# Kernel optimization log

Hardware: AMD Instinct MI355X
Metric: run time of the kernel (lower is better)

The kernel has to match this reference:

```python
import jax, jax.numpy as jnp
import numpy as np

N = 100000
E = 800000
HID = 128
HEADS = 4
NEG_SLOPE = 0.2


def _mlp2(x, w1, b1, w2, b2):
    h = jax.nn.relu(x @ w1.T + b1)
    return jax.nn.relu(h @ w2.T + b2)


def gat_conv(h, src, dst, lin_w, att_src, att_dst, bias, heads, out_ch, concat):
    # h: [N, in] -> hl: [N, heads, out_ch]
    n = h.shape[0]
    hl = (h @ lin_w.T).reshape(n, heads, out_ch)
    a_s = jnp.sum(hl * att_src, axis=-1)  # [N, heads]
    a_d = jnp.sum(hl * att_dst, axis=-1)
    alpha = jax.nn.leaky_relu(a_s[src] + a_d[dst], NEG_SLOPE)  # [E', heads]
    amax = jax.ops.segment_max(alpha, dst, num_segments=n)
    ex = jnp.exp(alpha - amax[dst])
    denom = jax.ops.segment_sum(ex, dst, num_segments=n)
    att = ex / denom[dst]  # segment softmax over incoming edges
    msg = hl[src] * att[:, :, None]  # [E', heads, out_ch]
    out = jax.ops.segment_sum(msg, dst, num_segments=n)
    out = out.reshape(n, heads * out_ch) if concat else out.mean(axis=1)
    return out + bias


def setup_inputs() -> dict:
    key = jax.random.key(0)
    ks = iter(jax.random.split(key, 40))
    g = lambda shape: (jax.random.normal(next(ks), shape, dtype=jnp.float32) * 0.1)
    inp = {}
    inp['x'] = jax.random.normal(next(ks), (N, 2), dtype=jnp.float32)
    inp['node_types'] = jax.random.randint(next(ks), (N,), 0, 2, dtype=jnp.int32)
    inp['edge_index'] = jax.random.randint(next(ks), (2, E), 0, N, dtype=jnp.int64)
    # heterogeneous encoder
    inp['ew1'] = g((HID, 2)); inp['eb1'] = g((HID,))
    inp['ew2'] = g((HID, HID)); inp['eb2'] = g((HID,))
    inp['cw1'] = g((HID, 1)); inp['cb1'] = g((HID,))
    inp['cw2'] = g((HID, HID)); inp['cb2'] = g((HID,))
    # GAT layers 0,1: heads=4, out_ch=HID//4, concat
    C = HID // HEADS
    inp['lin0'] = g((HID, HID)); inp['as0'] = g((HEADS, C)); inp['ad0'] = g((HEADS, C)); inp['b0'] = g((HID,))
    inp['lin1'] = g((HID, HID)); inp['as1'] = g((HEADS, C)); inp['ad1'] = g((HEADS, C)); inp['b1'] = g((HID,))
    # GAT layer 2: heads=1, out_ch=HID, concat=False
    inp['lin2'] = g((HID, HID)); inp['as2'] = g((1, HID)); inp['ad2'] = g((1, HID)); inp['b2'] = g((HID,))
    # decoder
    inp['dw1'] = g((HID, HID)); inp['db1'] = g((HID,))
    inp['dw2'] = g((HID // 2, HID)); inp['db2'] = g((HID // 2,))
    inp['dw3'] = g((1, HID // 2)); inp['db3'] = g((1,))
    return inp


def reference(x, node_types, edge_index, ew1, eb1, ew2, eb2, cw1, cb1, cw2, cb2,
              lin0, as0, ad0, b0, lin1, as1, ad1, b1, lin2, as2, ad2, b2,
              dw1, db1, dw2, db2, dw3, db3):
    n = x.shape[0]
    # heterogeneous encoding (vectorized type select)
    item_h = _mlp2(x[:, :2], ew1, eb1, ew2, eb2)
    con_h = _mlp2(x[:, :1], cw1, cb1, cw2, cb2)
    item_mask = node_types == 0
    h = jnp.where(item_mask[:, None], item_h, jnp.where((node_types == 1)[:, None], con_h, 0.0))
    # add self-loops (PyG GATConv default add_self_loops=True)
    loop = jnp.arange(n, dtype=edge_index.dtype)
    src = jnp.concatenate([edge_index[0], loop])
    dst = jnp.concatenate([edge_index[1], loop])
    C = HID // HEADS
    h0 = jax.nn.relu(gat_conv(h, src, dst, lin0, as0, ad0, b0, HEADS, C, True))
    h1 = h0 + jax.nn.relu(gat_conv(h0, src, dst, lin1, as1, ad1, b1, HEADS, C, True))
    h2 = h1 + jax.nn.relu(gat_conv(h1, src, dst, lin2, as2, ad2, b2, 1, HID, False))
    # decoder on all nodes; zero out non-item nodes (dropout is eval/no-op)
    d = jax.nn.relu(h2 @ dw1.T + db1)
    d = jax.nn.relu(d @ dw2.T + db2)
    probs = jax.nn.sigmoid(d @ dw3.T + db3).squeeze(-1)
    return probs * item_mask.astype(probs.dtype)
```

## Files before the change

kernel.cpp:

```cpp
#include <hip/hip_runtime.h>
#include <math.h>

#define HIDDEN 128
#define NEG_SLOPE 0.2f

typedef unsigned short u16;
typedef __attribute__((ext_vector_type(8))) short bf16x8;
typedef __attribute__((ext_vector_type(4))) float f32x4;

__device__ __forceinline__ u16 f2bf(float f) {
    unsigned u = __float_as_uint(f);
    unsigned r = (u + 0x7FFFu + ((u >> 16) & 1u)) >> 16;
    return (u16)r;
}
__device__ __forceinline__ float bf2f(u16 u) {
    return __uint_as_float((unsigned)u << 16);
}
__device__ __forceinline__ unsigned pack2(float a, float b) {
    return (unsigned)f2bf(a) | ((unsigned)f2bf(b) << 16);
}
__device__ __forceinline__ float lo16f(unsigned v) { return bf2f((u16)v); }
__device__ __forceinline__ float hi16f(unsigned v) { return bf2f((u16)(v >> 16)); }

struct WPtrs { const float* p[7]; };
__global__ void convw_zero_kernel(WPtrs wp, unsigned* __restrict__ wb, int totalPairs,
                                  int* __restrict__ cnt, int N) {
    int i = blockIdx.x * blockDim.x + threadIdx.x;
    if (i < N) cnt[i] = 0;
    if (i < totalPairs) {
        int e = i * 2;
        int seg, off;
        if (e < 98304) { seg = e >> 14; off = e & 16383; }
        else           { seg = 6;       off = e - 98304; }
        const float* s = wp.p[seg];
        wb[i] = pack2(s[off], s[off + 1]);
    }
}

__global__ __launch_bounds__(256) void encoder_kernel(
        const float* __restrict__ x, const int* __restrict__ types,
        const float* __restrict__ ew1, const float* __restrict__ eb1,
        const float* __restrict__ cw1, const float* __restrict__ cb1,
        const u16* __restrict__ wb_ew2, const u16* __restrict__ wb_cw2,
        const float* __restrict__ eb2, const float* __restrict__ cb2,
        u16* __restrict__ out, int N) {
    __shared__ u16 Ws[128 * 136];
    __shared__ float xsh[128];
    __shared__ float w1sh[640];
    const int tid = threadIdx.x;
    const int n0 = blockIdx.x * 64;

    if (tid < 128) {
        int n = n0 + (tid >> 1);
        xsh[tid] = (n < N) ? x[2 * n + (tid & 1)] : 0.f;
    }
    if (tid < 256) w1sh[tid] = ew1[tid];
    if (tid < 128) { w1sh[256 + tid] = eb1[tid]; w1sh[384 + tid] = cw1[tid];
                     w1sh[512 + tid] = cb1[tid]; }
#pragma unroll
    for (int r = 0; r < 8; r++) {
        int j = r * 256 + tid;
        int row = j >> 4, c8 = (j & 15) << 3;
        *(uint4*)&Ws[row * 136 + c8] = *(const uint4*)&wb_ew2[(size_t)row * 128 + c8];
    }
    __syncthreads();

    const int w = tid >> 6, lane = tid & 63;
    const int qd = lane >> 4, lr = lane & 15;
    const int row = w * 16 + lr;
    const float x0 = xsh[2 * row], x1 = xsh[2 * row + 1];

    f32x4 acc_i[8], acc_c[8];
#pragma unroll
    for (int j = 0; j < 8; j++) acc_i[j] = (f32x4){0.f, 0.f, 0.f, 0.f};

#pragma unroll
    for (int k = 0; k < 4; k++) {
        bf16x8 a;
#pragma unroll
        for (int j = 0; j < 8; j++) {
            int t = k * 32 + qd * 8 + j;
            float v = fmaxf(w1sh[2 * t] * x0 + w1sh[2 * t + 1] * x1 + w1sh[256 + t], 0.f);
            a[j] = (short)f2bf(v);
        }
#pragma unroll
        for (int j = 0; j < 8; j++) {
            bf16x8 b = *(const bf16x8*)&Ws[(j * 16 + lr) * 136 + k * 32 + qd * 8];
            acc_i[j] = __builtin_amdgcn_mfma_f32_16x16x32_bf16(a, b, acc_i[j], 0, 0, 0);
        }
    }
    __syncthreads();

#pragma unroll
    for (int r = 0; r < 8; r++) {
        int j = r * 256 + tid;
        int rw = j >> 4, c8 = (j & 15) << 3;
        *(uint4*)&Ws[rw * 136 + c8] = *(const uint4*)&wb_cw2[(size_t)rw * 128 + c8];
    }
    __syncthreads();

#pragma unroll
    for (int j = 0; j < 8; j++) acc_c[j] = (f32x4){0.f, 0.f, 0.f, 0.f};
#pragma unroll
    for (int k = 0; k < 4; k++) {
        bf16x8 a;
#pragma unroll
        for (int j = 0; j < 8; j++) {
            int t = k * 32 + qd * 8 + j;
            float v = fmaxf(w1sh[384 + t] * x0 + w1sh[512 + t], 0.f);
            a[j] = (short)f2bf(v);
        }
#pragma unroll
        for (int j = 0; j < 8; j++) {
            bf16x8 b = *(const bf16x8*)&Ws[(j * 16 + lr) * 136 + k * 32 + qd * 8];
            acc_c[j] = __builtin_amdgcn_mfma_f32_16x16x32_bf16(a, b, acc_c[j], 0, 0, 0);
        }
    }

#pragma unroll
    for (int r = 0; r < 4; r++) {
        int orow = n0 + w * 16 + qd * 4 + r;
        if (orow >= N) continue;
        int ty = types[orow];
#pragma unroll
        for (int j = 0; j < 8; j++) {
            int col = j * 16 + lr;
            float v;
            if (ty == 0)      v = fmaxf(acc_i[j][r] + eb2[col], 0.f);
            else if (ty == 1) v = fmaxf(acc_c[j][r] + cb2[col], 0.f);
            else              v = 0.f;
            out[(size_t)orow * HIDDEN + col] = f2bf(v);
        }
    }
}

template <int OUT, int DH>
__global__ __launch_bounds__(256) void gemm_mfma_kernel(
        const u16* __restrict__ X, const u16* __restrict__ Wb,
        const float* __restrict__ bias, const int* __restrict__ types,
        u16* __restrict__ out, float* __restrict__ a_s, float* __restrict__ a_d,
        const float* __restrict__ att_s, const float* __restrict__ att_d,
        const float* __restrict__ dw3, const float* __restrict__ db3,
        float* __restrict__ fout, int N, int mode) {
    constexpr int NT = OUT / 16;
    __shared__ u16 Xs[64 * 136];
    __shared__ u16 Ws[OUT * 136];
    const int tid = threadIdx.x;
    const int n0 = blockIdx.x * 64;

#pragma unroll
    for (int r = 0; r < 4; r++) {
        int j = r * 256 + tid;
        int row = j >> 4, c8 = (j & 15) << 3;
        int n = n0 + row;
        uint4 v = make_uint4(0u, 0u, 0u, 0u);
        if (n < N) v = *(const uint4*)&X[(size_t)n * 128 + c8];
        *(uint4*)&Xs[row * 136 + c8] = v;
    }
#pragma unroll
    for (int r = 0; r < NT; r++) {
        int j = r * 256 + tid;
        int row = j >> 4, c8 = (j & 15) << 3;
        *(uint4*)&Ws[row * 136 + c8] = *(const uint4*)&Wb[(size_t)row * 128 + c8];
    }
    __syncthreads();

    const int w = tid >> 6, lane = tid & 63;
    const int qd = lane >> 4, lr = lane & 15;

    f32x4 acc[NT];
#pragma unroll
    for (int j = 0; j < NT; j++) acc[j] = (f32x4){0.f, 0.f, 0.f, 0.f};

#pragma unroll
    for (int k = 0; k < 4; k++) {
        bf16x8 a = *(const bf16x8*)&Xs[(w * 16 + lr) * 136 + k * 32 + qd * 8];
#pragma unroll
        for (int j = 0; j < NT; j++) {
            bf16x8 b = *(const bf16x8*)&Ws[(j * 16 + lr) * 136 + k * 32 + qd * 8];
            acc[j] = __builtin_amdgcn_mfma_f32_16x16x32_bf16(a, b, acc[j], 0, 0, 0);
        }
    }

    if (mode == 3) {
        float pr[4] = {0.f, 0.f, 0.f, 0.f};
#pragma unroll
        for (int j = 0; j < NT; j++) {
            int col = j * 16 + lr;
            float b = bias[col], wv = dw3[col];
#pragma unroll
            for (int r = 0; r < 4; r++) pr[r] += fmaxf(acc[j][r] + b, 0.f) * wv;
        }
#pragma unroll
        for (int m = 1; m < 16; m <<= 1)
#pragma unroll
            for (int r = 0; r < 4; r++) pr[r] += __shfl_xor(pr[r], m, 64);
        if (lr == 0) {
            float b3 = db3[0];
#pragma unroll
            for (int r = 0; r < 4; r++) {
                int row = n0 + w * 16 + qd * 4 + r;
                if (row < N) {
                    float prob = 1.f / (1.f + expf(-(pr[r] + b3)));
                    fout[row] = (types[row] == 0) ? prob : 0.f;
                }
            }
        }
        return;
    }

    if (DH > 0) {
        constexpr int NH = (DH == 4) ? 4 : 1;
        float sp[NH][4], dp[NH][4];
#pragma unroll
        for (int h = 0; h < NH; h++)
#pragma unroll
            for (int r = 0; r < 4; r++) { sp[h][r] = 0.f; dp[h][r] = 0.f; }
#pragma unroll
        for (int j = 0; j < NT; j++) {
            int col = j * 16 + lr;
            float as_ = att_s[col], ad_ = att_d[col];
            int h = (DH == 4) ? (j >> 1) : 0;
#pragma unroll
            for (int r = 0; r < 4; r++) {
                sp[h][r] += acc[j][r] * as_;
                dp[h][r] += acc[j][r] * ad_;
            }
        }
#pragma unroll
        for (int m = 1; m < 16; m <<= 1)
#pragma unroll
            for (int h = 0; h < NH; h++)
#pragma unroll
                for (int r = 0; r < 4; r++) {
                    sp[h][r] += __shfl_xor(sp[h][r], m, 64);
                    dp[h][r] += __shfl_xor(dp[h][r], m, 64);
                }
        if (lr == 0) {
#pragma unroll
            for (int r = 0; r < 4; r++) {
                int row = n0 + w * 16 + qd * 4 + r;
                if (row < N) {
#pragma unroll
                    for (int h = 0; h < NH; h++) {
                        a_s[row * DH + h] = sp[h][r];
                        a_d[row * DH + h] = dp[h][r];
                    }
                }
            }
        }
    }

#pragma unroll
    for (int r = 0; r < 4; r++) {
        int row = n0 + w * 16 + qd * 4 + r;
        if (row >= N) continue;
#pragma unroll
        for (int j = 0; j < NT; j++) {
            int col = j * 16 + lr;
            float v = acc[j][r];
            if (mode >= 1) v = fmaxf(v + bias[col], 0.f);
            out[(size_t)row * OUT + col] = f2bf(v);
        }
    }
}

__global__ void hist_kernel(const int* __restrict__ ei, int E, int E2,
                            int* __restrict__ cnt, int* __restrict__ pos) {
    int e = blockIdx.x * blockDim.x + threadIdx.x;
    if (e >= E2) return;
    int d = (e < E) ? ei[E + e] : e - E;
    pos[e] = atomicAdd(&cnt[d], 1);
}

__global__ void scan1_kernel(const int* __restrict__ cnt, int* __restrict__ rs,
                             int* __restrict__ bsum, int N) {
    __shared__ int s[256];
    int i = blockIdx.x * 256 + threadIdx.x;
    int v = (i < N) ? cnt[i] : 0;
    s[threadIdx.x] = v;
    __syncthreads();
    for (int off = 1; off < 256; off <<= 1) {
        int t = (threadIdx.x >= off) ? s[threadIdx.x - off] : 0;
        __syncthreads();
        s[threadIdx.x] += t;
        __syncthreads();
    }
    if (i < N) rs[i] = s[threadIdx.x];
    if (threadIdx.x == 255) bsum[blockIdx.x] = s[255];
}

__global__ void scan23_kernel(int* __restrict__ rs, const int* __restrict__ cnt,
                              const int* __restrict__ bsum, int N) {
    __shared__ int sdata[256];
    int b = blockIdx.x;
    int partial = 0;
    for (int i = threadIdx.x; i < b; i += 256) partial += bsum[i];
    sdata[threadIdx.x] = partial;
    __syncthreads();
    for (int off = 128; off; off >>= 1) {
        if (threadIdx.x < off) sdata[threadIdx.x] += sdata[threadIdx.x + off];
        __syncthreads();
    }
    int pre = sdata[0];
    int i = b * 256 + threadIdx.x;
    if (i < N) rs[i] = rs[i] - cnt[i] + pre;
}

__global__ void scatter_kernel(const int* __restrict__ ei, int E, int E2,
                               const int* __restrict__ rs, const int* __restrict__ pos,
                               int* __restrict__ srclist) {
    int e = blockIdx.x * blockDim.x + threadIdx.x;
    if (e >= E2) return;
    int s, d;
    if (e < E) { s = ei[e]; d = ei[E + e]; }
    else       { s = d = e - E; }
    srclist[rs[d] + pos[e]] = s;
}

template <int H>
__global__ __launch_bounds__(256) void gat_agg_kernel(
        const int* __restrict__ rs, const int* __restrict__ cnt,
        const int* __restrict__ srclist, const u16* __restrict__ hl,
        const float* __restrict__ a_s, const float* __restrict__ a_d,
        const float* __restrict__ bias, const u16* __restrict__ res,
        u16* __restrict__ out, int N) {
    int n = blockIdx.x * 4 + (threadIdx.x >> 6);
    int l = threadIdx.x & 63;
    if (n >= N) return;
    const int g = l >> 4;
    const int c = l & 15;
    const int head = (H == 1) ? 0 : (c >> 2);
    const int beg = rs[n];
    const int deg = cnt[n];
    const float ad = a_d[n * H + head];
    float acc0[8], acc1[8], acc2[8];
    float den0 = 0.f, den1 = 0.f, den2 = 0.f;
#pragma unroll
    for (int j = 0; j < 8; j++) { acc0[j] = 0.f; acc1[j] = 0.f; acc2[j] = 0.f; }

    for (int k = 0; k < deg; k += 12) {
        int i0 = k + g, i1 = k + 4 + g, i2 = k + 8 + g;
        int e0 = beg + min(i0, deg - 1);
        int e1 = beg + min(i1, deg - 1);
        int e2 = beg + min(i2, deg - 1);
        int s0 = srclist[e0], s1 = srclist[e1], s2 = srclist[e2];
        float al0 = a_s[s0 * H + head] + ad;
        float al1 = a_s[s1 * H + head] + ad;
        float al2 = a_s[s2 * H + head] + ad;
        al0 = (al0 > 0.f) ? al0 : NEG_SLOPE * al0;
        al1 = (al1 > 0.f) ? al1 : NEG_SLOPE * al1;
        al2 = (al2 > 0.f) ? al2 : NEG_SLOPE * al2;
        float p0 = __expf(fminf(al0, 80.f));
        float p1 = __expf(fminf(al1, 80.f));
        float p2 = __expf(fminf(al2, 80.f));
        if (i0 >= deg) p0 = 0.f;
        if (i1 >= deg) p1 = 0.f;
        if (i2 >= deg) p2 = 0.f;
        den0 += p0; den1 += p1; den2 += p2;
        uint4 v0 = *(const uint4*)&hl[(size_t)s0 * 128 + 8 * c];
        uint4 v1 = *(const uint4*)&hl[(size_t)s1 * 128 + 8 * c];
        uint4 v2 = *(const uint4*)&hl[(size_t)s2 * 128 + 8 * c];
        acc0[0] += p0 * lo16f(v0.x); acc0[1] += p0 * hi16f(v0.x);
        acc0[2] += p0 * lo16f(v0.y); acc0[3] += p0 * hi16f(v0.y);
        acc0[4] += p0 * lo16f(v0.z); acc0[5] += p0 * hi16f(v0.z);
        acc0[6] += p0 * lo16f(v0.w); acc0[7] += p0 * hi16f(v0.w);
        acc1[0] += p1 * lo16f(v1.x); acc1[1] += p1 * hi16f(v1.x);
        acc1[2] += p1 * lo16f(v1.y); acc1[3] += p1 * hi16f(v1.y);
        acc1[4] += p1 * lo16f(v1.z); acc1[5] += p1 * hi16f(v1.z);
        acc1[6] += p1 * lo16f(v1.w); acc1[7] += p1 * hi16f(v1.w);
        acc2[0] += p2 * lo16f(v2.x); acc2[1] += p2 * hi16f(v2.x);
        acc2[2] += p2 * lo16f(v2.y); acc2[3] += p2 * hi16f(v2.y);
        acc2[4] += p2 * lo16f(v2.z); acc2[5] += p2 * hi16f(v2.z);
        acc2[6] += p2 * lo16f(v2.w); acc2[7] += p2 * hi16f(v2.w);
    }
#pragma unroll
    for (int j = 0; j < 8; j++) {
        float a = acc0[j] + acc1[j] + acc2[j];
        a += __shfl_xor(a, 16, 64);
        a += __shfl_xor(a, 32, 64);
        acc0[j] = a;
    }
    float den = den0 + den1 + den2;
    den += __shfl_xor(den, 16, 64);
    den += __shfl_xor(den, 32, 64);
    if (g == 0) {
        float di = 1.f / den;
        float4 b0 = *(const float4*)&bias[8 * c];
        float4 b1 = *(const float4*)&bias[8 * c + 4];
        float o[8];
        o[0] = fmaxf(acc0[0] * di + b0.x, 0.f);
        o[1] = fmaxf(acc0[1] * di + b0.y, 0.f);
        o[2] = fmaxf(acc0[2] * di + b0.z, 0.f);
        o[3] = fmaxf(acc0[3] * di + b0.w, 0.f);
        o[4] = fmaxf(acc0[4] * di + b1.x, 0.f);
        o[5] = fmaxf(acc0[5] * di + b1.y, 0.f);
        o[6] = fmaxf(acc0[6] * di + b1.z, 0.f);
        o[7] = fmaxf(acc0[7] * di + b1.w, 0.f);
        if (res) {
            uint4 rv = *(const uint4*)&res[(size_t)n * 128 + 8 * c];
            o[0] += lo16f(rv.x); o[1] += hi16f(rv.x);
            o[2] += lo16f(rv.y); o[3] += hi16f(rv.y);
            o[4] += lo16f(rv.z); o[5] += hi16f(rv.z);
            o[6] += lo16f(rv.w); o[7] += hi16f(rv.w);
        }
        uint4 ov = make_uint4(pack2(o[0], o[1]), pack2(o[2], o[3]),
                              pack2(o[4], o[5]), pack2(o[6], o[7]));
        *(uint4*)&out[(size_t)n * 128 + 8 * c] = ov;
    }
}

template <int H>
static void gat_layer(const u16* X, const u16* lin, const float* as_, const float* ad_,
                      const float* bias, const u16* res, u16* hl, u16* outb,
                      float* a_s, float* a_d,
                      const int* rs, const int* cnt, const int* srclist,
                      int N, hipStream_t stream) {
    int gx = (N + 63) / 64;
    gemm_mfma_kernel<128, H><<<gx, 256, 0, stream>>>(
        X, lin, nullptr, nullptr, hl, a_s, a_d, as_, ad_, nullptr, nullptr, nullptr, N, 0);
    gat_agg_kernel<H><<<(N + 3) / 4, 256, 0, stream>>>(rs, cnt, srclist, hl, a_s, a_d,
                                                       bias, res, outb, N);
}

extern "C" void kernel_launch(void* const* d_in, const int* in_sizes, int n_in,
                              void* d_out, int out_size, void* d_ws, size_t ws_size,
                              hipStream_t stream) {
    const float* x     = (const float*)d_in[0];
    const int*   types = (const int*)d_in[1];
    const int*   ei    = (const int*)d_in[2];
    const float* ew1 = (const float*)d_in[3];
    const float* eb1 = (const float*)d_in[4];
    const float* ew2 = (const float*)d_in[5];
    const float* eb2 = (const float*)d_in[6];
    const float* cw1 = (const float*)d_in[7];
    const float* cb1 = (const float*)d_in[8];
    const float* cw2 = (const float*)d_in[9];
    const float* cb2 = (const float*)d_in[10];
    const float* lin0 = (const float*)d_in[11];
    const float* as0  = (const float*)d_in[12];
    const float* ad0  = (const float*)d_in[13];
    const float* b0   = (const float*)d_in[14];
    const float* lin1 = (const float*)d_in[15];
    const float* as1  = (const float*)d_in[16];
    const float* ad1  = (const float*)d_in[17];
    const float* b1   = (const float*)d_in[18];
    const float* lin2 = (const float*)d_in[19];
    const float* as2  = (const float*)d_in[20];
    const float* ad2  = (const float*)d_in[21];
    const float* b2   = (const float*)d_in[22];
    const float* dw1 = (const float*)d_in[23];
    const float* db1 = (const float*)d_in[24];
    const float* dw2 = (const float*)d_in[25];
    const float* db2 = (const float*)d_in[26];
    const float* dw3 = (const float*)d_in[27];
    const float* db3 = (const float*)d_in[28];

    int N  = in_sizes[1];
    int E  = in_sizes[2] / 2;
    int E2 = E + N;

    size_t NF = (size_t)N * HIDDEN;
    u16* bufA = (u16*)d_ws;
    u16* bufB = bufA + NF;
    u16* bufC = bufB + NF;
    float* fbase = (float*)(bufC + NF);
    float* a_s  = fbase;
    float* a_d  = a_s + (size_t)N * 4;
    int* rs      = (int*)(a_d + (size_t)N * 4);
    int* cnt     = rs + N;
    int* pos     = cnt + N;
    int* bsum    = pos + E2;
    int* srclist = bsum + 1024;
    u16* wb      = (u16*)(srclist + E2);
    u16* wb_ew2  = wb;
    u16* wb_cw2  = wb + 16384;
    u16* wb_lin0 = wb + 32768;
    u16* wb_lin1 = wb + 49152;
    u16* wb_lin2 = wb + 65536;
    u16* wb_dw1  = wb + 81920;
    u16* wb_dw2  = wb + 98304;

    int nb = (N + 255) / 256;

    WPtrs wp;
    wp.p[0] = ew2; wp.p[1] = cw2; wp.p[2] = lin0; wp.p[3] = lin1;
    wp.p[4] = lin2; wp.p[5] = dw1; wp.p[6] = dw2;
    int cz = max(N, 53248);
    convw_zero_kernel<<<(cz + 255) / 256, 256, 0, stream>>>(wp, (unsigned*)wb, 53248,
                                                            cnt, N);

    hist_kernel<<<(E2 + 255) / 256, 256, 0, stream>>>(ei, E, E2, cnt, pos);
    scan1_kernel<<<nb, 256, 0, stream>>>(cnt, rs, bsum, N);
    scan23_kernel<<<nb, 256, 0, stream>>>(rs, cnt, bsum, N);
    scatter_kernel<<<(E2 + 255) / 256, 256, 0, stream>>>(ei, E, E2, rs, pos, srclist);

    int gx = (N + 63) / 64;

    encoder_kernel<<<gx, 256, 0, stream>>>(x, types, ew1, eb1, cw1, cb1,
                                           wb_ew2, wb_cw2, eb2, cb2, bufA, N);

    gat_layer<4>(bufA, wb_lin0, as0, ad0, b0, nullptr, bufB, bufA,
                 a_s, a_d, rs, cnt, srclist, N, stream);
    gat_layer<4>(bufA, wb_lin1, as1, ad1, b1, bufA, bufB, bufC,
                 a_s, a_d, rs, cnt, srclist, N, stream);
    gat_layer<1>(bufC, wb_lin2, as2, ad2, b2, bufC, bufB, bufA,
                 a_s, a_d, rs, cnt, srclist, N, stream);

    gemm_mfma_kernel<128, 0><<<gx, 256, 0, stream>>>(
        bufA, wb_dw1, db1, nullptr, bufC, nullptr, nullptr, nullptr, nullptr,
        nullptr, nullptr, nullptr, N, 1);
    gemm_mfma_kernel<64, 0><<<gx, 256, 0, stream>>>(
        bufC, wb_dw2, db2, types, nullptr, nullptr, nullptr, nullptr, nullptr,
        dw3, db3, (float*)d_out, N, 3);
}
```

Before: 483.6 us.

## Fuse encoder with first GAT linear and fuse two decoder GEMMs

The encoder MLP output is kept in shared memory and fed directly into the layer-0 GAT projection and attention-logit computation, so the intermediate node features are no longer written to and re-read from global memory. The two decoder GEMMs plus the final sigmoid are merged into one kernel, with the hidden activations staged in LDS. This removes two kernel launches and two full N×128 bf16 round trips. In exchange, the fused kernels use more LDS and registers per block, which may lower occupancy.

```diff
diff --git a/kernel.cpp b/kernel.cpp
--- a/kernel.cpp
+++ b/kernel.cpp
@@ -37,14 +37,18 @@
     }
 }
 
-__global__ __launch_bounds__(256) void encoder_kernel(
+__global__ __launch_bounds__(256) void enc_gemm_kernel(
         const float* __restrict__ x, const int* __restrict__ types,
         const float* __restrict__ ew1, const float* __restrict__ eb1,
         const float* __restrict__ cw1, const float* __restrict__ cb1,
         const u16* __restrict__ wb_ew2, const u16* __restrict__ wb_cw2,
         const float* __restrict__ eb2, const float* __restrict__ cb2,
-        u16* __restrict__ out, int N) {
+        const u16* __restrict__ wb_lin0,
+        const float* __restrict__ att_s, const float* __restrict__ att_d,
+        u16* __restrict__ hl, float* __restrict__ a_s, float* __restrict__ a_d,
+        int N) {
     __shared__ u16 Ws[128 * 136];
+    __shared__ u16 Xs[64 * 136];
     __shared__ float xsh[128];
     __shared__ float w1sh[640];
     const int tid = threadIdx.x;
@@ -67,8 +71,8 @@
 
     const int w = tid >> 6, lane = tid & 63;
     const int qd = lane >> 4, lr = lane & 15;
-    const int row = w * 16 + lr;
-    const float x0 = xsh[2 * row], x1 = xsh[2 * row + 1];
+    const int arow = w * 16 + lr;
+    const float x0 = xsh[2 * arow], x1 = xsh[2 * arow + 1];
 
     f32x4 acc_i[8], acc_c[8];
 #pragma unroll
@@ -90,7 +94,6 @@
         }
     }
     __syncthreads();
-
 #pragma unroll
     for (int r = 0; r < 8; r++) {
         int j = r * 256 + tid;
@@ -119,9 +122,9 @@
 
 #pragma unroll
     for (int r = 0; r < 4; r++) {
-        int orow = n0 + w * 16 + qd * 4 + r;
-        if (orow >= N) continue;
-        int ty = types[orow];
+        int drow = w * 16 + qd * 4 + r;
+        int orow = n0 + drow;
+        int ty = (orow < N) ? types[orow] : 2;
 #pragma unroll
         for (int j = 0; j < 8; j++) {
             int col = j * 16 + lr;
@@ -129,22 +132,89 @@
             if (ty == 0)      v = fmaxf(acc_i[j][r] + eb2[col], 0.f);
             else if (ty == 1) v = fmaxf(acc_c[j][r] + cb2[col], 0.f);
             else              v = 0.f;
-            out[(size_t)orow * HIDDEN + col] = f2bf(v);
-        }
-    }
-}
-
-template <int OUT, int DH>
-__global__ __launch_bounds__(256) void gemm_mfma_kernel(
+            float vo = __shfl_xor(v, 1, 64);
+            if ((lr & 1) == 0)
+                *(unsigned*)&Xs[drow * 136 + j * 16 + lr] = pack2(v, vo);
+        }
+    }
+    __syncthreads();
+#pragma unroll
+    for (int r = 0; r < 8; r++) {
+        int j = r * 256 + tid;
+        int rw = j >> 4, c8 = (j & 15) << 3;
+        *(uint4*)&Ws[rw * 136 + c8] = *(const uint4*)&wb_lin0[(size_t)rw * 128 + c8];
+    }
+    __syncthreads();
+
+    f32x4 acc[8];
+#pragma unroll
+    for (int j = 0; j < 8; j++) acc[j] = (f32x4){0.f, 0.f, 0.f, 0.f};
+#pragma unroll
+    for (int k = 0; k < 4; k++) {
+        bf16x8 a = *(const bf16x8*)&Xs[arow * 136 + k * 32 + qd * 8];
+#pragma unroll
+        for (int j = 0; j < 8; j++) {
+            bf16x8 b = *(const bf16x8*)&Ws[(j * 16 + lr) * 136 + k * 32 + qd * 8];
+            acc[j] = __builtin_amdgcn_mfma_f32_16x16x32_bf16(a, b, acc[j], 0, 0, 0);
+        }
+    }
+
+    float sp[4][4], dp[4][4];
+#pragma unroll
+    for (int h = 0; h < 4; h++)
+#pragma unroll
+        for (int r = 0; r < 4; r++) { sp[h][r] = 0.f; dp[h][r] = 0.f; }
+#pragma unroll
+    for (int j = 0; j < 8; j++) {
+        int col = j * 16 + lr;
+        float as_ = att_s[col], ad_ = att_d[col];
+        int h = j >> 1;
+#pragma unroll
+        for (int r = 0; r < 4; r++) {
+            sp[h][r] += acc[j][r] * as_;
+            dp[h][r] += acc[j][r] * ad_;
+        }
+    }
+#pragma unroll
+    for (int m = 1; m < 16; m <<= 1)
+#pragma unroll
+        for (int h = 0; h < 4; h++)
+#pragma unroll
+            for (int r = 0; r < 4; r++) {
+                sp[h][r] += __shfl_xor(sp[h][r], m, 64);
+                dp[h][r] += __shfl_xor(dp[h][r], m, 64);
+            }
+    if (lr == 0) {
+#pragma unroll
+        for (int r = 0; r < 4; r++) {
+            int row = n0 + w * 16 + qd * 4 + r;
+            if (row < N) {
+#pragma unroll
+                for (int h = 0; h < 4; h++) {
+                    a_s[row * 4 + h] = sp[h][r];
+                    a_d[row * 4 + h] = dp[h][r];
+                }
+            }
+        }
+    }
+#pragma unroll
+    for (int r = 0; r < 4; r++) {
+        int row = n0 + w * 16 + qd * 4 + r;
+        if (row >= N) continue;
+#pragma unroll
+        for (int j = 0; j < 8; j++)
+            hl[(size_t)row * 128 + j * 16 + lr] = f2bf(acc[j][r]);
+    }
+}
+
+template <int DH>
+__global__ __launch_bounds__(256) void gemm_hl_kernel(
         const u16* __restrict__ X, const u16* __restrict__ Wb,
-        const float* __restrict__ bias, const int* __restrict__ types,
-        u16* __restrict__ out, float* __restrict__ a_s, float* __restrict__ a_d,
         const float* __restrict__ att_s, const float* __restrict__ att_d,
-        const float* __restrict__ dw3, const float* __restrict__ db3,
-        float* __restrict__ fout, int N, int mode) {
-    constexpr int NT = OUT / 16;
+        u16* __restrict__ hl, float* __restrict__ a_s, float* __restrict__ a_d,
+        int N) {
     __shared__ u16 Xs[64 * 136];
-    __shared__ u16 Ws[OUT * 136];
+    __shared__ u16 Ws[128 * 136];
     const int tid = threadIdx.x;
     const int n0 = blockIdx.x * 64;
 
@@ -158,7 +228,7 @@
         *(uint4*)&Xs[row * 136 + c8] = v;
     }
 #pragma unroll
-    for (int r = 0; r < NT; r++) {
+    for (int r = 0; r < 8; r++) {
         int j = r * 256 + tid;
         int row = j >> 4, c8 = (j & 15) << 3;
         *(uint4*)&Ws[row * 136 + c8] = *(const uint4*)&Wb[(size_t)row * 128 + c8];
@@ -168,99 +238,166 @@
     const int w = tid >> 6, lane = tid & 63;
     const int qd = lane >> 4, lr = lane & 15;
 
-    f32x4 acc[NT];
-#pragma unroll
-    for (int j = 0; j < NT; j++) acc[j] = (f32x4){0.f, 0.f, 0.f, 0.f};
-
+    f32x4 acc[8];
+#pragma unroll
+    for (int j = 0; j < 8; j++) acc[j] = (f32x4){0.f, 0.f, 0.f, 0.f};
 #pragma unroll
     for (int k = 0; k < 4; k++) {
         bf16x8 a = *(const bf16x8*)&Xs[(w * 16 + lr) * 136 + k * 32 + qd * 8];
 #pragma unroll
-        for (int j = 0; j < NT; j++) {
+        for (int j = 0; j < 8; j++) {
             bf16x8 b = *(const bf16x8*)&Ws[(j * 16 + lr) * 136 + k * 32 + qd * 8];
             acc[j] = __builtin_amdgcn_mfma_f32_16x16x32_bf16(a, b, acc[j], 0, 0, 0);
         }
     }
 
-    if (mode == 3) {
-        float pr[4] = {0.f, 0.f, 0.f, 0.f};
-#pragma unroll
-        for (int j = 0; j < NT; j++) {
-            int col = j * 16 + lr;
-            float b = bias[col], wv = dw3[col];
-#pragma unroll
-            for (int r = 0; r < 4; r++) pr[r] += fmaxf(acc[j][r] + b, 0.f) * wv;
-        }
-#pragma unroll
-        for (int m = 1; m < 16; m <<= 1)
-#pragma unroll
-            for (int r = 0; r < 4; r++) pr[r] += __shfl_xor(pr[r], m, 64);
-        if (lr == 0) {
-            float b3 = db3[0];
+    constexpr int NH = (DH == 4) ? 4 : 1;
+    float sp[NH][4], dp[NH][4];
+#pragma unroll
+    for (int h = 0; h < NH; h++)
+#pragma unroll
+        for (int r = 0; r < 4; r++) { sp[h][r] = 0.f; dp[h][r] = 0.f; }
+#pragma unroll
+    for (int j = 0; j < 8; j++) {
+        int col = j * 16 + lr;
+        float as_ = att_s[col], ad_ = att_d[col];
+        int h = (DH == 4) ? (j >> 1) : 0;
+#pragma unroll
+        for (int r = 0; r < 4; r++) {
+            sp[h][r] += acc[j][r] * as_;
+            dp[h][r] += acc[j][r] * ad_;
+        }
+    }
+#pragma unroll
+    for (int m = 1; m < 16; m <<= 1)
+#pragma unroll
+        for (int h = 0; h < NH; h++)
 #pragma unroll
             for (int r = 0; r < 4; r++) {
-                int row = n0 + w * 16 + qd * 4 + r;
-                if (row < N) {
-                    float prob = 1.f / (1.f + expf(-(pr[r] + b3)));
-                    fout[row] = (types[row] == 0) ? prob : 0.f;
+                sp[h][r] += __shfl_xor(sp[h][r], m, 64);
+                dp[h][r] += __shfl_xor(dp[h][r], m, 64);
+            }
+    if (lr == 0) {
+#pragma unroll
+        for (int r = 0; r < 4; r++) {
+            int row = n0 + w * 16 + qd * 4 + r;
+            if (row < N) {
+#pragma unroll
+                for (int h = 0; h < NH; h++) {
+                    a_s[row * DH + h] = sp[h][r];
+                    a_d[row * DH + h] = dp[h][r];
                 }
             }
         }
-        return;
-    }
-
-    if (DH > 0) {
-        constexpr int NH = (DH == 4) ? 4 : 1;
-        float sp[NH][4], dp[NH][4];
-#pragma unroll
-        for (int h = 0; h < NH; h++)
-#pragma unroll
-            for (int r = 0; r < 4; r++) { sp[h][r] = 0.f; dp[h][r] = 0.f; }
-#pragma unroll
-        for (int j = 0; j < NT; j++) {
-            int col = j * 16 + lr;
-            float as_ = att_s[col], ad_ = att_d[col];
-            int h = (DH == 4) ? (j >> 1) : 0;
-#pragma unroll
-            for (int r = 0; r < 4; r++) {
-                sp[h][r] += acc[j][r] * as_;
-                dp[h][r] += acc[j][r] * ad_;
-            }
-        }
-#pragma unroll
-        for (int m = 1; m < 16; m <<= 1)
-#pragma unroll
-            for (int h = 0; h < NH; h++)
-#pragma unroll
-                for (int r = 0; r < 4; r++) {
-                    sp[h][r] += __shfl_xor(sp[h][r], m, 64);
-                    dp[h][r] += __shfl_xor(dp[h][r], m, 64);
-                }
-        if (lr == 0) {
-#pragma unroll
-            for (int r = 0; r < 4; r++) {
-                int row = n0 + w * 16 + qd * 4 + r;
-                if (row < N) {
-#pragma unroll
-                    for (int h = 0; h < NH; h++) {
-                        a_s[row * DH + h] = sp[h][r];
-                        a_d[row * DH + h] = dp[h][r];
-                    }
-                }
-            }
-        }
-    }
-
+    }
 #pragma unroll
     for (int r = 0; r < 4; r++) {
         int row = n0 + w * 16 + qd * 4 + r;
         if (row >= N) continue;
 #pragma unroll
-        for (int j = 0; j < NT; j++) {
+        for (int j = 0; j < 8; j++)
+            hl[(size_t)row * 128 + j * 16 + lr] = f2bf(acc[j][r]);
+    }
+}
+
+__global__ __launch_bounds__(256) void dec_kernel(
+        const u16* __restrict__ X, const int* __restrict__ types,
+        const u16* __restrict__ wb_dw1, const float* __restrict__ db1,
+        const u16* __restrict__ wb_dw2, const float* __restrict__ db2,
+        const float* __restrict__ dw3, const float* __restrict__ db3,
+        float* __restrict__ fout, int N) {
+    __shared__ u16 Xs[64 * 136];
+    __shared__ u16 Ws[128 * 136];
+    const int tid = threadIdx.x;
+    const int n0 = blockIdx.x * 64;
+
+#pragma unroll
+    for (int r = 0; r < 4; r++) {
+        int j = r * 256 + tid;
+        int row = j >> 4, c8 = (j & 15) << 3;
+        int n = n0 + row;
+        uint4 v = make_uint4(0u, 0u, 0u, 0u);
+        if (n < N) v = *(const uint4*)&X[(size_t)n * 128 + c8];
+        *(uint4*)&Xs[row * 136 + c8] = v;
+    }
+#pragma unroll
+    for (int r = 0; r < 8; r++) {
+        int j = r * 256 + tid;
+        int row = j >> 4, c8 = (j & 15) << 3;
+        *(uint4*)&Ws[row * 136 + c8] = *(const uint4*)&wb_dw1[(size_t)row * 128 + c8];
+    }
+    __syncthreads();
+
+    const int w = tid >> 6, lane = tid & 63;
+    const int qd = lane >> 4, lr = lane & 15;
+
+    f32x4 acc[8];
+#pragma unroll
+    for (int j = 0; j < 8; j++) acc[j] = (f32x4){0.f, 0.f, 0.f, 0.f};
+#pragma unroll
+    for (int k = 0; k < 4; k++) {
+        bf16x8 a = *(const bf16x8*)&Xs[(w * 16 + lr) * 136 + k * 32 + qd * 8];
+#pragma unroll
+        for (int j = 0; j < 8; j++) {
+            bf16x8 b = *(const bf16x8*)&Ws[(j * 16 + lr) * 136 + k * 32 + qd * 8];
+            acc[j] = __builtin_amdgcn_mfma_f32_16x16x32_bf16(a, b, acc[j], 0, 0, 0);
+        }
+    }
+    __syncthreads();
+
+#pragma unroll
+    for (int r = 0; r < 4; r++) {
+        int drow = w * 16 + qd * 4 + r;
+#pragma unroll
+        for (int j = 0; j < 8; j++) {
             int col = j * 16 + lr;
-            float v = acc[j][r];
-            if (mode >= 1) v = fmaxf(v + bias[col], 0.f);
-            out[(size_t)row * OUT + col] = f2bf(v);
+            float v = fmaxf(acc[j][r] + db1[col], 0.f);
+            float vo = __shfl_xor(v, 1, 64);
+            if ((lr & 1) == 0)
+                *(unsigned*)&Xs[drow * 136 + j * 16 + lr] = pack2(v, vo);
+        }
+    }
+#pragma unroll
+    for (int r = 0; r < 4; r++) {
+        int j = r * 256 + tid;
+        int row = j >> 4, c8 = (j & 15) << 3;
+        *(uint4*)&Ws[row * 136 + c8] = *(const uint4*)&wb_dw2[(size_t)row * 128 + c8];
+    }
+    __syncthreads();
+
+    f32x4 acc2[4];
+#pragma unroll
+    for (int j = 0; j < 4; j++) acc2[j] = (f32x4){0.f, 0.f, 0.f, 0.f};
+#pragma unroll
+    for (int k = 0; k < 4; k++) {
+        bf16x8 a = *(const bf16x8*)&Xs[(w * 16 + lr) * 136 + k * 32 + qd * 8];
+#pragma unroll
+        for (int j = 0; j < 4; j++) {
+            bf16x8 b = *(const bf16x8*)&Ws[(j * 16 + lr) * 136 + k * 32 + qd * 8];
+            acc2[j] = __builtin_amdgcn_mfma_f32_16x16x32_bf16(a, b, acc2[j], 0, 0, 0);
+        }
+    }
+    float pr[4] = {0.f, 0.f, 0.f, 0.f};
+#pragma unroll
+    for (int j = 0; j < 4; j++) {
+        int col = j * 16 + lr;
+        float b = db2[col], wv = dw3[col];
+#pragma unroll
+        for (int r = 0; r < 4; r++) pr[r] += fmaxf(acc2[j][r] + b, 0.f) * wv;
+    }
+#pragma unroll
+    for (int m = 1; m < 16; m <<= 1)
+#pragma unroll
+        for (int r = 0; r < 4; r++) pr[r] += __shfl_xor(pr[r], m, 64);
+    if (lr == 0) {
+        float b3 = db3[0];
+#pragma unroll
+        for (int r = 0; r < 4; r++) {
+            int row = n0 + w * 16 + qd * 4 + r;
+            if (row < N) {
+                float prob = 1.f / (1.f + expf(-(pr[r] + b3)));
+                fout[row] = (types[row] == 0) ? prob : 0.f;
+            }
         }
     }
 }
@@ -410,19 +547,6 @@
     }
 }
 
-template <int H>
-static void gat_layer(const u16* X, const u16* lin, const float* as_, const float* ad_,
-                      const float* bias, const u16* res, u16* hl, u16* outb,
-                      float* a_s, float* a_d,
-                      const int* rs, const int* cnt, const int* srclist,
-                      int N, hipStream_t stream) {
-    int gx = (N + 63) / 64;
-    gemm_mfma_kernel<128, H><<<gx, 256, 0, stream>>>(
-        X, lin, nullptr, nullptr, hl, a_s, a_d, as_, ad_, nullptr, nullptr, nullptr, N, 0);
-    gat_agg_kernel<H><<<(N + 3) / 4, 256, 0, stream>>>(rs, cnt, srclist, hl, a_s, a_d,
-                                                       bias, res, outb, N);
-}
-
 extern "C" void kernel_launch(void* const* d_in, const int* in_sizes, int n_in,
                               void* d_out, int out_size, void* d_ws, size_t ws_size,
                               hipStream_t stream) {
@@ -464,8 +588,7 @@
     u16* bufA = (u16*)d_ws;
     u16* bufB = bufA + NF;
     u16* bufC = bufB + NF;
-    float* fbase = (float*)(bufC + NF);
-    float* a_s  = fbase;
+    float* a_s  = (float*)(bufC + NF);
     float* a_d  = a_s + (size_t)N * 4;
     int* rs      = (int*)(a_d + (size_t)N * 4);
     int* cnt     = rs + N;
@@ -497,20 +620,20 @@
 
     int gx = (N + 63) / 64;
 
-    encoder_kernel<<<gx, 256, 0, stream>>>(x, types, ew1, eb1, cw1, cb1,
-                                           wb_ew2, wb_cw2, eb2, cb2, bufA, N);
-
-    gat_layer<4>(bufA, wb_lin0, as0, ad0, b0, nullptr, bufB, bufA,
-                 a_s, a_d, rs, cnt, srclist, N, stream);
-    gat_layer<4>(bufA, wb_lin1, as1, ad1, b1, bufA, bufB, bufC,
-                 a_s, a_d, rs, cnt, srclist, N, stream);
-    gat_layer<1>(bufC, wb_lin2, as2, ad2, b2, bufC, bufB, bufA,
-                 a_s, a_d, rs, cnt, srclist, N, stream);
-
-    gemm_mfma_kernel<128, 0><<<gx, 256, 0, stream>>>(
-        bufA, wb_dw1, db1, nullptr, bufC, nullptr, nullptr, nullptr, nullptr,
-        nullptr, nullptr, nullptr, N, 1);
-    gemm_mfma_kernel<64, 0><<<gx, 256, 0, stream>>>(
-        bufC, wb_dw2, db2, types, nullptr, nullptr, nullptr, nullptr, nullptr,
-        dw3, db3, (float*)d_out, N, 3);
-}
+    enc_gemm_kernel<<<gx, 256, 0, stream>>>(x, types, ew1, eb1, cw1, cb1,
+                                            wb_ew2, wb_cw2, eb2, cb2, wb_lin0,
+                                            as0, ad0, bufB, a_s, a_d, N);
+    gat_agg_kernel<4><<<(N + 3) / 4, 256, 0, stream>>>(rs, cnt, srclist, bufB,
+                                                       a_s, a_d, b0, nullptr, bufA, N);
+    gemm_hl_kernel<4><<<gx, 256, 0, stream>>>(bufA, wb_lin1, as1, ad1,
+                                              bufB, a_s, a_d, N);
+    gat_agg_kernel<4><<<(N + 3) / 4, 256, 0, stream>>>(rs, cnt, srclist, bufB,
+                                                       a_s, a_d, b1, bufA, bufC, N);
+    gemm_hl_kernel<1><<<gx, 256, 0, stream>>>(bufC, wb_lin2, as2, ad2,
+                                              bufB, a_s, a_d, N);
+    gat_agg_kernel<1><<<(N + 3) / 4, 256, 0, stream>>>(rs, cnt, srclist, bufB,
+                                                       a_s, a_d, b2, bufC, bufA, N);
+
+    dec_kernel<<<gx, 256, 0, stream>>>(bufA, types, wb_dw1, db1, wb_dw2, db2,
+                                       dw3, db3, (float*)d_out, N);
+}
```

New measurement: 462.9 us. 1.04x faster.
